# Optimization experiments

Hardware: AMD Instinct MI355X
Metric: run time of the kernel (lower is better)

The kernel has to match this reference:

```python
import math
import jax, jax.numpy as jnp
import numpy as np

EPS = 1e-12

def _layernorm(x, g, b):
    u = x.mean(-1, keepdims=True)
    s = ((x - u) ** 2).mean(-1, keepdims=True)
    return g * (x - u) / jnp.sqrt(s + EPS) + b

def _sinusoidal_pe(S, d):
    pos = np.arange(S, dtype=np.float32)[:, None]
    div = np.exp(np.arange(0, d, 2, dtype=np.float32) * -(math.log(10000.0) / d))
    pe = np.zeros((S, d), dtype=np.float32)
    pe[:, 0::2] = np.sin(pos * div)
    pe[:, 1::2] = np.cos(pos * div)
    return jnp.asarray(pe)

def setup_inputs() -> dict:
    key = jax.random.key(0)
    k1, k2, k3, k4 = jax.random.split(key, 4)
    B, L, V, Dw, H = 32, 2048, 30522, 300, 768
    P = 16                      # separator period -> S = L // P ingredients per row
    S = L // P
    ids = jax.random.randint(k1, (B, L), 1, V).astype(jnp.int32)
    sep = np.zeros((B, L), dtype=np.int32)
    sep[:, P - 1::P] = 1        # a separator token every P tokens
    emb_table = jax.random.normal(k2, (V, Dw), dtype=jnp.float32) * 0.02
    emb_table = emb_table.at[0].set(0.0)  # padding_idx=0
    W = jax.random.normal(k3, (Dw, H), dtype=jnp.float32) * 0.02
    b = jnp.zeros((H,), dtype=jnp.float32)
    return {
        "ingr_input_ids": ids,
        "ingr_sep_masks": jnp.asarray(sep),
        "num_ingr": S,
        "emb_table": emb_table,
        "ln1_g": jnp.ones((Dw,), jnp.float32),
        "ln1_b": jnp.zeros((Dw,), jnp.float32),
        "W": W,
        "b": b,
        "ln2_g": jnp.ones((H,), jnp.float32),
        "ln2_b": jnp.zeros((H,), jnp.float32),
    }

def reference(ingr_input_ids, ingr_sep_masks, num_ingr,
              emb_table, ln1_g, ln1_b, W, b, ln2_g, ln2_b):
    S = int(num_ingr)
    H = W.shape[1]
    # embed + LN + Linear + ReLU + LN (dropout is identity at eval)
    e = emb_table[ingr_input_ids]                       # [B, L, Dw]
    h = _layernorm(e, ln1_g, ln1_b)
    h = jax.nn.relu(jnp.einsum('bld,dh->blh', h, W) + b)
    h = _layernorm(h, ln2_g, ln2_b)                     # [B, L, H]
    # ragged segment mean: segment id = exclusive cumsum of sep mask;
    # separator tokens (out[:-1] in the original) are excluded from the mean;
    # tokens after the last separator fall into bucket S and are dropped.
    sep = ingr_sep_masks
    seg = jnp.cumsum(sep, axis=1) - sep                 # [B, L]
    seg = jnp.minimum(seg, S)
    valid = (1 - sep).astype(h.dtype)                   # [B, L]
    seg_sum = jax.vmap(lambda hh, ss: jax.ops.segment_sum(hh, ss, num_segments=S + 1))(
        h * valid[..., None], seg)                      # [B, S+1, H]
    seg_cnt = jax.vmap(lambda vv, ss: jax.ops.segment_sum(vv, ss, num_segments=S + 1))(
        valid, seg)                                     # [B, S+1]
    mean = jnp.where(seg_cnt[..., None] > 0,
                     seg_sum / jnp.maximum(seg_cnt, 1.0)[..., None],
                     0.0)[:, :S]                        # [B, S, H]
    return mean + _sinusoidal_pe(S, H)[None]
```

## Files before the change

### kernel.cpp

```cpp
#include <hip/hip_runtime.h>
#include <hip/hip_bf16.h>

#define B_   32
#define L_   2048
#define V_   30522
#define DW   300
#define H_   768
#define KP   320
#define NT   (H_/16)
#define KT   (KP/32)
#define VPAD 30528
#define MB   64
#define NMT  4
#define NW   6
#define APAD 336

typedef __attribute__((ext_vector_type(8))) short bf16x8;
typedef __attribute__((ext_vector_type(4))) float f32x4;

__global__ void setup(const float* __restrict__ W, __hip_bfloat16* __restrict__ Wp,
                      float* __restrict__ PE, int peBlocks, int S,
                      const int* __restrict__ sep, int* __restrict__ pos,
                      int* __restrict__ nsep) {
    __shared__ int cnt[256];
    int bid = blockIdx.x;
    if (bid < 120) {
        int t = bid * 256 + threadIdx.x;
        int lane = t & 63;
        int f    = t >> 6;
        int n    = f % NT;
        int kt   = f / NT;
        int col  = n * 16 + (lane & 15);
        int k0   = kt * 32 + (lane >> 4) * 8;
        union { __hip_bfloat16 h[8]; int4 v; } u;
        #pragma unroll
        for (int j = 0; j < 8; ++j) {
            int k = k0 + j;
            float w = (k < DW) ? W[(size_t)k * H_ + col] : 0.f;
            u.h[j] = __float2bfloat16(w);
        }
        reinterpret_cast<int4*>(Wp)[t] = u.v;
    } else if (bid < 120 + peBlocks) {
        int t = (bid - 120) * 256 + threadIdx.x;
        if (t < S * H_) {
            int s = t / H_, n = t % H_;
            const float cexp = -9.210340371976184f / (float)H_;
            float div = expf((float)(2 * (n >> 1)) * cexp);
            float ang = (float)s * div;
            PE[t] = (n & 1) ? cosf(ang) : sinf(ang);
        }
    } else {
        int b = bid - 120 - peBlocks;
        const int* row = sep + (size_t)b * L_;
        int tid = threadIdx.x;
        int local[8]; int c = 0;
        #pragma unroll
        for (int i = 0; i < 8; ++i) { int v = row[tid * 8 + i]; local[i] = v; c += v; }
        cnt[tid] = c; __syncthreads();
        for (int ofs = 1; ofs < 256; ofs <<= 1) {
            int v = (tid >= ofs) ? cnt[tid - ofs] : 0;
            __syncthreads();
            cnt[tid] += v;
            __syncthreads();
        }
        int w = cnt[tid] - c;
        #pragma unroll
        for (int i = 0; i < 8; ++i)
            if (local[i]) { pos[(size_t)b * L_ + w] = tid * 8 + i; ++w; }
        if (tid == 255) nsep[b] = cnt[255];
    }
}

__global__ void __launch_bounds__(512, 2)
gemm_ln2(const float* __restrict__ emb, const float* __restrict__ g1,
         const float* __restrict__ b1, const __hip_bfloat16* __restrict__ Wp,
         const float* __restrict__ bias, const float* __restrict__ g2,
         const float* __restrict__ b2, __hip_bfloat16* __restrict__ G) {
    __shared__ __hip_bfloat16 sA[MB * APAD];
    __shared__ float sred[2][8][MB];
    int tid  = threadIdx.x;
    int w    = tid >> 6;
    int lane = tid & 63;
    int r = lane & 15, q = lane >> 4;
    size_t row0 = (size_t)blockIdx.x * MB;

    const bf16x8* Bv = reinterpret_cast<const bf16x8*>(Wp) + (size_t)w * NW * 64 + lane;
    int phase = (int)(blockIdx.x % KT);

    bf16x8 bbuf[2][NW];
    bf16x8 abuf[2][NMT];

    {
        const bf16x8* bp = Bv + (size_t)phase * NT * 64;
        #pragma unroll
        for (int nl = 0; nl < NW; ++nl) bbuf[0][nl] = bp[nl * 64];
    }

    {
        float g1v[5], b1v[5];
        #pragma unroll
        for (int i = 0; i < 5; ++i) {
            int k = lane + i * 64;
            g1v[i] = (k < DW) ? g1[k] : 0.f;
            b1v[i] = (k < DW) ? b1[k] : 0.f;
        }
        #pragma unroll
        for (int rr = 0; rr < 8; ++rr) {
            int lrow = w * 8 + rr;
            size_t gvr = row0 + lrow;
            __hip_bfloat16* dst = &sA[lrow * APAD];
            if (gvr < V_) {
                const float* rowp = emb + gvr * (size_t)DW;
                float x[5]; float s = 0.f, ssum = 0.f;
                #pragma unroll
                for (int i = 0; i < 5; ++i) {
                    int k = lane + i * 64;
                    float v = (k < DW) ? rowp[k] : 0.f;
                    x[i] = v; s += v; ssum += v * v;
                }
                #pragma unroll
                for (int m = 32; m >= 1; m >>= 1) { s += __shfl_xor(s, m); ssum += __shfl_xor(ssum, m); }
                float mu   = s / (float)DW;
                float var  = ssum / (float)DW - mu * mu;
                float rstd = rsqrtf(var + 1e-12f);
                #pragma unroll
                for (int i = 0; i < 5; ++i) {
                    int k = lane + i * 64;
                    float o = (k < DW) ? (g1v[i] * ((x[i] - mu) * rstd) + b1v[i]) : 0.f;
                    dst[k] = __float2bfloat16(o);
                }
            } else {
                for (int k = lane; k < KP; k += 64) dst[k] = __float2bfloat16(0.f);
            }
        }
    }

    f32x4 acc[NW][NMT];
    #pragma unroll
    for (int nl = 0; nl < NW; ++nl)
        #pragma unroll
        for (int m = 0; m < NMT; ++m) acc[nl][m] = (f32x4){0.f, 0.f, 0.f, 0.f};

    const char* sAc = reinterpret_cast<const char*>(sA);
    const int abase = r * (APAD * 2) + q * 16;

    __syncthreads();
    #pragma unroll
    for (int m = 0; m < NMT; ++m)
        abuf[0][m] = *reinterpret_cast<const bf16x8*>(
            sAc + abase + m * (16 * APAD * 2) + phase * 64);

    #pragma unroll
    for (int i = 0; i < KT; ++i) {
        const int cur = i & 1, nxt = (i + 1) & 1;
        if (i + 1 < KT) {
            int ktn = phase + i + 1; if (ktn >= KT) ktn -= KT;
            const bf16x8* bp = Bv + (size_t)ktn * NT * 64;
            #pragma unroll
            for (int nl = 0; nl < NW; ++nl) bbuf[nxt][nl] = bp[nl * 64];
            #pragma unroll
            for (int m = 0; m < NMT; ++m)
                abuf[nxt][m] = *reinterpret_cast<const bf16x8*>(
                    sAc + abase + m * (16 * APAD * 2) + ktn * 64);
        }
        __builtin_amdgcn_sched_barrier(0);
        __builtin_amdgcn_s_setprio(1);
        #pragma unroll
        for (int nl = 0; nl < NW; ++nl) {
            acc[nl][0] = __builtin_amdgcn_mfma_f32_16x16x32_bf16(abuf[cur][0], bbuf[cur][nl], acc[nl][0], 0, 0, 0);
            acc[nl][1] = __builtin_amdgcn_mfma_f32_16x16x32_bf16(abuf[cur][1], bbuf[cur][nl], acc[nl][1], 0, 0, 0);
            acc[nl][2] = __builtin_amdgcn_mfma_f32_16x16x32_bf16(abuf[cur][2], bbuf[cur][nl], acc[nl][2], 0, 0, 0);
            acc[nl][3] = __builtin_amdgcn_mfma_f32_16x16x32_bf16(abuf[cur][3], bbuf[cur][nl], acc[nl][3], 0, 0, 0);
        }
        __builtin_amdgcn_s_setprio(0);
    }

    float s_[NMT][4], ss_[NMT][4];
    #pragma unroll
    for (int m = 0; m < NMT; ++m)
        #pragma unroll
        for (int j = 0; j < 4; ++j) { s_[m][j] = 0.f; ss_[m][j] = 0.f; }
    #pragma unroll
    for (int nl = 0; nl < NW; ++nl) {
        float bn = bias[w * 96 + nl * 16 + r];
        #pragma unroll
        for (int m = 0; m < NMT; ++m)
            #pragma unroll
            for (int j = 0; j < 4; ++j) {
                float v = acc[nl][m][j] + bn;
                v = v > 0.f ? v : 0.f;
                acc[nl][m][j] = v;
                s_[m][j] += v; ss_[m][j] += v * v;
            }
    }
    #pragma unroll
    for (int msk = 1; msk < 16; msk <<= 1)
        #pragma unroll
        for (int m = 0; m < NMT; ++m)
            #pragma unroll
            for (int j = 0; j < 4; ++j) {
                s_[m][j]  += __shfl_xor(s_[m][j],  msk);
                ss_[m][j] += __shfl_xor(ss_[m][j], msk);
            }
    if (r == 0) {
        #pragma unroll
        for (int m = 0; m < NMT; ++m)
            #pragma unroll
            for (int j = 0; j < 4; ++j) {
                int row = m * 16 + q * 4 + j;
                sred[0][w][row] = s_[m][j];
                sred[1][w][row] = ss_[m][j];
            }
    }
    __syncthreads();

    #pragma unroll
    for (int m = 0; m < NMT; ++m) {
        #pragma unroll
        for (int j = 0; j < 4; ++j) {
            int row = m * 16 + q * 4 + j;
            float ts = 0.f, tss = 0.f;
            #pragma unroll
            for (int ww = 0; ww < 8; ++ww) { ts += sred[0][ww][row]; tss += sred[1][ww][row]; }
            float mu   = ts / (float)H_;
            float var  = tss / (float)H_ - mu * mu;
            float rstd = rsqrtf(var + 1e-12f);
            s_[m][j]  = mu;
            ss_[m][j] = rstd;
        }
    }
    #pragma unroll
    for (int nl = 0; nl < NW; ++nl) {
        int col = w * 96 + nl * 16 + r;
        float gg = g2[col], bb = b2[col];
        #pragma unroll
        for (int m = 0; m < NMT; ++m)
            #pragma unroll
            for (int j = 0; j < 4; ++j) {
                size_t rowg = row0 + m * 16 + q * 4 + j;
                float val = gg * (acc[nl][m][j] - s_[m][j]) * ss_[m][j] + bb;
                G[rowg * H_ + col] = __float2bfloat16(val);
            }
    }
}

__global__ void seg_gather(const int* __restrict__ ids, const int* __restrict__ pos,
                           const int* __restrict__ nsep, const __hip_bfloat16* __restrict__ G,
                           const float* __restrict__ PE, float* __restrict__ out, int S) {
    int blk = blockIdx.x;
    int s = blk % S, b = blk / S;
    int tid = threadIdx.x;
    int g = tid / 96;
    int l = tid % 96;
    int ns = nsep[b];
    int lo, hi;
    if (s > ns) { lo = 1; hi = 0; }
    else {
        lo = (s == 0) ? 0 : pos[(size_t)b * L_ + (s - 1)] + 1;
        hi = (s < ns) ? pos[(size_t)b * L_ + s] - 1 : L_ - 1;
    }
    int cnt = hi - lo + 1; if (cnt < 0) cnt = 0;

    float a[8] = {0.f, 0.f, 0.f, 0.f, 0.f, 0.f, 0.f, 0.f};
    for (int t = lo + g; t <= hi; t += 4) {
        int v = ids[(size_t)b * L_ + t];
        int4 raw = *reinterpret_cast<const int4*>(G + (size_t)v * H_ + l * 8);
        const unsigned short* u = reinterpret_cast<const unsigned short*>(&raw);
        #pragma unroll
        for (int k = 0; k < 8; ++k) {
            union { unsigned int i; float f; } c; c.i = ((unsigned int)u[k]) << 16;
            a[k] += c.f;
        }
    }
    __shared__ float red[3][96 * 8];
    if (g > 0) {
        #pragma unroll
        for (int k = 0; k < 8; ++k) red[g - 1][l * 8 + k] = a[k];
    }
    __syncthreads();
    if (g == 0) {
        float inv = (cnt > 0) ? 1.f / (float)cnt : 0.f;
        float* orow = out + ((size_t)b * S + s) * H_;
        const float* pe = PE + (size_t)s * H_;
        #pragma unroll
        for (int k = 0; k < 8; ++k) {
            int n = l * 8 + k;
            float tot = a[k] + red[0][l * 8 + k] + red[1][l * 8 + k] + red[2][l * 8 + k];
            orow[n] = tot * inv + pe[n];
        }
    }
}

extern "C" void kernel_launch(void* const* d_in, const int* in_sizes, int n_in,
                              void* d_out, int out_size, void* d_ws, size_t ws_size,
                              hipStream_t stream) {
    const int*   ids  = (const int*)d_in[0];
    const int*   sep  = (const int*)d_in[1];
    const float* emb  = (const float*)d_in[3];
    const float* g1   = (const float*)d_in[4];
    const float* b1   = (const float*)d_in[5];
    const float* W    = (const float*)d_in[6];
    const float* bias = (const float*)d_in[7];
    const float* g2   = (const float*)d_in[8];
    const float* b2   = (const float*)d_in[9];
    float* out = (float*)d_out;

    int S = out_size / (B_ * H_);

    char* ws = (char*)d_ws;
    __hip_bfloat16* Wp  = (__hip_bfloat16*)(ws);
    __hip_bfloat16* G   = (__hip_bfloat16*)(ws + 491520);
    int*   pos  = (int*)(ws + 491520 + 46891008);
    int*   nsep = (int*)(ws + 491520 + 46891008 + 262144);
    float* PE   = (float*)(ws + 491520 + 46891008 + 262144 + 256);
    (void)ws_size; (void)n_in; (void)in_sizes;

    int peBlocks = (S * H_ + 255) / 256;
    setup    <<<120 + peBlocks + B_, 256, 0, stream>>>(W, Wp, PE, peBlocks, S, sep, pos, nsep);
    gemm_ln2 <<<VPAD / MB, 512, 0, stream>>>(emb, g1, b1, Wp, bias, g2, b2, G);
    seg_gather<<<B_ * S, 384, 0, stream>>>(ids, pos, nsep, G, PE, out, S);
}
```

Baseline: 72.49 us.

## Halve GEMM row tile, stage embedding rows via coalesced float4 LDS loads

Reduces the per-block row tile from 64 to 32 rows and raises launch bounds to 4 blocks per CU to increase occupancy and parallelism across the vocabulary-sized GEMM. Embedding rows are now copied into shared memory with flat coalesced float4 loads before LayerNorm, which is then computed from LDS with vectorized packed bf16 stores. The A-fragment register double buffer is dropped in favor of loading A directly from LDS each k-step, cutting register pressure. The extra raw-float LDS buffer raises shared memory per block and halves reuse of each B fragment.

```diff
diff --git a/kernel.cpp b/kernel.cpp
--- a/kernel.cpp
+++ b/kernel.cpp
@@ -10,8 +10,8 @@
 #define NT   (H_/16)
 #define KT   (KP/32)
 #define VPAD 30528
-#define MB   64
-#define NMT  4
+#define MB   32
+#define NMT  2
 #define NW   6
 #define APAD 336
 
@@ -71,11 +71,12 @@
     }
 }
 
-__global__ void __launch_bounds__(512, 2)
+__global__ void __launch_bounds__(512, 4)
 gemm_ln2(const float* __restrict__ emb, const float* __restrict__ g1,
          const float* __restrict__ b1, const __hip_bfloat16* __restrict__ Wp,
          const float* __restrict__ bias, const float* __restrict__ g2,
          const float* __restrict__ b2, __hip_bfloat16* __restrict__ G) {
+    __shared__ float sRaw[MB * DW];
     __shared__ __hip_bfloat16 sA[MB * APAD];
     __shared__ float sred[2][8][MB];
     int tid  = threadIdx.x;
@@ -88,7 +89,6 @@
     int phase = (int)(blockIdx.x % KT);
 
     bf16x8 bbuf[2][NW];
-    bf16x8 abuf[2][NMT];
 
     {
         const bf16x8* bp = Bv + (size_t)phase * NT * 64;
@@ -97,40 +97,65 @@
     }
 
     {
-        float g1v[5], b1v[5];
+        const float4* esrc = reinterpret_cast<const float4*>(emb + row0 * DW);
+        long validf4 = ((long)V_ * DW) / 4 - (long)(row0 * DW) / 4;
+        int lim = (validf4 > (long)(MB * DW / 4)) ? (MB * DW / 4) : (int)validf4;
         #pragma unroll
         for (int i = 0; i < 5; ++i) {
-            int k = lane + i * 64;
-            g1v[i] = (k < DW) ? g1[k] : 0.f;
-            b1v[i] = (k < DW) ? b1[k] : 0.f;
-        }
-        #pragma unroll
-        for (int rr = 0; rr < 8; ++rr) {
-            int lrow = w * 8 + rr;
-            size_t gvr = row0 + lrow;
+            int j = tid + i * 512;
+            if (j < MB * DW / 4) {
+                float4 v;
+                if (j < lim) v = esrc[j];
+                else { v.x = 0.f; v.y = 0.f; v.z = 0.f; v.w = 0.f; }
+                *reinterpret_cast<float4*>(&sRaw[j * 4]) = v;
+            }
+        }
+    }
+    __syncthreads();
+
+    {
+        int k0 = lane << 2;
+        int k1 = k0 + 256;
+        bool val1 = (k1 + 3 < DW);
+        float4 g1a = *reinterpret_cast<const float4*>(g1 + k0);
+        float4 b1a = *reinterpret_cast<const float4*>(b1 + k0);
+        float4 g1b, b1b;
+        if (val1) {
+            g1b = *reinterpret_cast<const float4*>(g1 + k1);
+            b1b = *reinterpret_cast<const float4*>(b1 + k1);
+        } else { g1b.x=g1b.y=g1b.z=g1b.w=0.f; b1b.x=b1b.y=b1b.z=b1b.w=0.f; }
+        #pragma unroll
+        for (int rr = 0; rr < 4; ++rr) {
+            int lrow = w * 4 + rr;
+            const float* rp = &sRaw[(size_t)lrow * DW];
+            float4 v0 = *reinterpret_cast<const float4*>(rp + k0);
+            float4 v1;
+            if (val1) v1 = *reinterpret_cast<const float4*>(rp + k1);
+            else { v1.x=0.f; v1.y=0.f; v1.z=0.f; v1.w=0.f; }
+            float s  = v0.x + v0.y + v0.z + v0.w + v1.x + v1.y + v1.z + v1.w;
+            float ss = v0.x*v0.x + v0.y*v0.y + v0.z*v0.z + v0.w*v0.w
+                     + v1.x*v1.x + v1.y*v1.y + v1.z*v1.z + v1.w*v1.w;
+            #pragma unroll
+            for (int m = 32; m >= 1; m >>= 1) { s += __shfl_xor(s, m); ss += __shfl_xor(ss, m); }
+            float mu   = s / (float)DW;
+            float var  = ss / (float)DW - mu * mu;
+            float rstd = rsqrtf(var + 1e-12f);
             __hip_bfloat16* dst = &sA[lrow * APAD];
-            if (gvr < V_) {
-                const float* rowp = emb + gvr * (size_t)DW;
-                float x[5]; float s = 0.f, ssum = 0.f;
-                #pragma unroll
-                for (int i = 0; i < 5; ++i) {
-                    int k = lane + i * 64;
-                    float v = (k < DW) ? rowp[k] : 0.f;
-                    x[i] = v; s += v; ssum += v * v;
-                }
-                #pragma unroll
-                for (int m = 32; m >= 1; m >>= 1) { s += __shfl_xor(s, m); ssum += __shfl_xor(ssum, m); }
-                float mu   = s / (float)DW;
-                float var  = ssum / (float)DW - mu * mu;
-                float rstd = rsqrtf(var + 1e-12f);
-                #pragma unroll
-                for (int i = 0; i < 5; ++i) {
-                    int k = lane + i * 64;
-                    float o = (k < DW) ? (g1v[i] * ((x[i] - mu) * rstd) + b1v[i]) : 0.f;
-                    dst[k] = __float2bfloat16(o);
-                }
-            } else {
-                for (int k = lane; k < KP; k += 64) dst[k] = __float2bfloat16(0.f);
+            union { __hip_bfloat16 h[4]; uint2 u2; } p0;
+            p0.h[0] = __float2bfloat16(g1a.x * ((v0.x - mu) * rstd) + b1a.x);
+            p0.h[1] = __float2bfloat16(g1a.y * ((v0.y - mu) * rstd) + b1a.y);
+            p0.h[2] = __float2bfloat16(g1a.z * ((v0.z - mu) * rstd) + b1a.z);
+            p0.h[3] = __float2bfloat16(g1a.w * ((v0.w - mu) * rstd) + b1a.w);
+            *reinterpret_cast<uint2*>(&dst[k0]) = p0.u2;
+            if (k1 < KP) {
+                union { __hip_bfloat16 h[4]; uint2 u2; } p1;
+                if (val1) {
+                    p1.h[0] = __float2bfloat16(g1b.x * ((v1.x - mu) * rstd) + b1b.x);
+                    p1.h[1] = __float2bfloat16(g1b.y * ((v1.y - mu) * rstd) + b1b.y);
+                    p1.h[2] = __float2bfloat16(g1b.z * ((v1.z - mu) * rstd) + b1b.z);
+                    p1.h[3] = __float2bfloat16(g1b.w * ((v1.w - mu) * rstd) + b1b.w);
+                } else { p1.u2.x = 0u; p1.u2.y = 0u; }
+                *reinterpret_cast<uint2*>(&dst[k1]) = p1.u2;
             }
         }
     }
@@ -145,32 +170,25 @@
     const int abase = r * (APAD * 2) + q * 16;
 
     __syncthreads();
-    #pragma unroll
-    for (int m = 0; m < NMT; ++m)
-        abuf[0][m] = *reinterpret_cast<const bf16x8*>(
-            sAc + abase + m * (16 * APAD * 2) + phase * 64);
 
     #pragma unroll
     for (int i = 0; i < KT; ++i) {
         const int cur = i & 1, nxt = (i + 1) & 1;
+        int kt = phase + i; if (kt >= KT) kt -= KT;
         if (i + 1 < KT) {
             int ktn = phase + i + 1; if (ktn >= KT) ktn -= KT;
             const bf16x8* bp = Bv + (size_t)ktn * NT * 64;
             #pragma unroll
             for (int nl = 0; nl < NW; ++nl) bbuf[nxt][nl] = bp[nl * 64];
-            #pragma unroll
-            for (int m = 0; m < NMT; ++m)
-                abuf[nxt][m] = *reinterpret_cast<const bf16x8*>(
-                    sAc + abase + m * (16 * APAD * 2) + ktn * 64);
         }
         __builtin_amdgcn_sched_barrier(0);
+        bf16x8 a0 = *reinterpret_cast<const bf16x8*>(sAc + abase + kt * 64);
+        bf16x8 a1 = *reinterpret_cast<const bf16x8*>(sAc + abase + 16 * APAD * 2 + kt * 64);
         __builtin_amdgcn_s_setprio(1);
         #pragma unroll
         for (int nl = 0; nl < NW; ++nl) {
-            acc[nl][0] = __builtin_amdgcn_mfma_f32_16x16x32_bf16(abuf[cur][0], bbuf[cur][nl], acc[nl][0], 0, 0, 0);
-            acc[nl][1] = __builtin_amdgcn_mfma_f32_16x16x32_bf16(abuf[cur][1], bbuf[cur][nl], acc[nl][1], 0, 0, 0);
-            acc[nl][2] = __builtin_amdgcn_mfma_f32_16x16x32_bf16(abuf[cur][2], bbuf[cur][nl], acc[nl][2], 0, 0, 0);
-            acc[nl][3] = __builtin_amdgcn_mfma_f32_16x16x32_bf16(abuf[cur][3], bbuf[cur][nl], acc[nl][3], 0, 0, 0);
+            acc[nl][0] = __builtin_amdgcn_mfma_f32_16x16x32_bf16(a0, bbuf[cur][nl], acc[nl][0], 0, 0, 0);
+            acc[nl][1] = __builtin_amdgcn_mfma_f32_16x16x32_bf16(a1, bbuf[cur][nl], acc[nl][1], 0, 0, 0);
         }
         __builtin_amdgcn_s_setprio(0);
     }
```

Result: no change. 71.45 us (-1.4%).
